# Optimization experiments

Hardware: AMD Instinct MI355X
Metric: run time of the kernel (lower is better)

## Reference

```python
import jax, jax.numpy as jnp
import numpy as np

SAMPLE_RATE = 16000
SOUND_SPEED = 343.0
MAX_ORDER = 15
RIR_LENGTH = 3968
WINDOW_LENGTH = 81
PAD = WINDOW_LENGTH // 2  # 40

# Static image-source lattice (depends only on max_order): all integer
# reflection index triplets with |nx|+|ny|+|nz| <= max_order.
_ind = np.arange(-MAX_ORDER, MAX_ORDER + 1)
_grid = np.stack(np.meshgrid(_ind, _ind, _ind, indexing="ij"), -1).reshape(-1, 3)
XYZ = _grid[np.abs(_grid).sum(1) <= MAX_ORDER].astype(np.float32)  # (I,3), I=4991
EXP_LO = np.abs(np.floor(XYZ / 2)).astype(np.float32)        # hits on lower walls per dim
EXP_HI = np.abs(np.floor((XYZ + 1) / 2)).astype(np.float32)  # hits on upper walls per dim


def _hann(x, T):
    # continuous Hann window sampled at non-integer points, zero outside |x|<=T/2
    return jnp.where(jnp.abs(x) <= T / 2, 0.5 * (1.0 + jnp.cos(2.0 * jnp.pi * x / T)), 0.0)


def _forward(inp):
    room = inp[:, 0:3]                 # (B,3) room dimensions [m]
    mic = inp[:, 3:6] * room           # (B,3)
    src = inp[:, 6:9] * room           # (B,3)
    a_w = inp[:, 9:10]
    absorption = jnp.concatenate([a_w, a_w, a_w, a_w, inp[:, 10:11], inp[:, 11:12]], axis=1)
    absorption = absorption * 0.84 + 0.01            # (B,6): [x-,x+,y-,y+,floor,ceiling]
    tr = jnp.sqrt(1.0 - absorption)                  # wall reflection coefficients

    xyz = jnp.asarray(XYZ)                           # (I,3)
    d = room[:, None, :]
    s = src[:, None, :]
    # image source locations (B,I,3): mirror parity per torchaudio ISM
    img_loc = jnp.where(xyz % 2 == 1, d * (xyz + 1.0) - s, d * xyz + s)
    # per-image-source attenuation (B,I)
    t_lo = tr[:, None, 0::2]                         # (B,1,3) lower walls per dim
    t_hi = tr[:, None, 1::2]                         # (B,1,3) upper walls per dim
    att = jnp.prod(t_lo ** jnp.asarray(EXP_LO) * t_hi ** jnp.asarray(EXP_HI), axis=-1)

    dist = jnp.linalg.norm(img_loc - mic[:, None, :], axis=-1)   # (B,I)
    amp = att / dist                                              # 1/r spreading
    delay = dist * (SAMPLE_RATE / SOUND_SPEED)                    # fractional sample delay
    delay_i = jnp.ceil(delay)

    # windowed-sinc fractional-delay pulse sampled at n = delay_i-PAD .. delay_i+PAD
    n_rel = jnp.arange(-PAD, PAD + 1, dtype=jnp.float32)          # (W,)
    x = delay_i[..., None] + n_rel - delay[..., None]             # (B,I,W)
    sig = amp[..., None] * jnp.sinc(x) * _hann(x, 2 * PAD)        # (B,I,W)

    # scatter-accumulate pulses at time index n, dropping out-of-range samples
    t_idx = (delay_i[..., None] + n_rel).astype(jnp.int32)        # (B,I,W)
    B = inp.shape[0]
    b_idx = jnp.arange(B, dtype=jnp.int32)[:, None, None]
    rir = jnp.zeros((B, RIR_LENGTH), dtype=sig.dtype).at[b_idx, t_idx].add(sig, mode="drop")

    toa = PAD + SAMPLE_RATE * jnp.linalg.norm(mic - src, axis=1) / SOUND_SPEED  # (B,)
    return rir, toa


def setup_inputs():
    key = jax.random.key(0)
    u = jax.random.uniform(key, (128, 12), dtype=jnp.float32)
    room = 2.0 + 8.0 * u[:, :3]          # room dims in [2,10] m
    rest = 0.05 + 0.9 * u[:, 3:]         # mic/src fractions and absorptions in (0,1)
    return {"input": jnp.concatenate([room, rest], axis=1)}


def reference(input):
    return _forward(input)
```

## Files before the change

### kernel.cpp

```cpp
#include <hip/hip_runtime.h>

#define NIMG    4991
#define RIRLEN  3968
#define NT      512
#define NGRP    8
#define KPT     10
#define INV_PI  0.31830988618379067f
#define SR_OVER_C 46.647230320699704f

struct Tab { int v[NIMG]; };
static constexpr Tab make_tab() {
    Tab t{};
    int k = 0;
    for (int x = -15; x <= 15; ++x)
        for (int y = -15; y <= 15; ++y)
            for (int z = -15; z <= 15; ++z) {
                int ax = x < 0 ? -x : x;
                int ay = y < 0 ? -y : y;
                int az = z < 0 ? -z : z;
                if (ax + ay + az <= 15)
                    t.v[k++] = (x + 15) | ((y + 15) << 8) | ((z + 15) << 16);
            }
    return t;
}
__constant__ Tab c_tab = make_tab();

static __device__ __forceinline__ int iabs(int v) { return v < 0 ? -v : v; }

typedef __fp16 f16x2 __attribute__((ext_vector_type(2)));

__global__ __launch_bounds__(NT, 4)
void rir_fused(const float* __restrict__ inp, float* __restrict__ out, int B) {
    const int bx   = blockIdx.x;
    const int b    = bx >> 3;
    const int g    = bx & 7;
    const int tid  = threadIdx.x;
    const int lane = tid & 63;
    const int wv   = tid >> 6;
    const int q    = lane & 3;

    __shared__ __align__(16) float2   s_dh[NIMG];
    __shared__ __align__(16) unsigned s_cs[NIMG];
    __shared__ float    s_par[12];
    __shared__ float    s_p2[3][32];
    __shared__ float    s_at[3][32];
    __shared__ int      s_h4[256][4];
    __shared__ int      s_off[257];
    __shared__ float    s_acc[8][64];

    for (int k = tid; k < 1024; k += NT) ((int*)s_h4)[k] = 0;
    if (tid < 512) ((float*)s_acc)[tid] = 0.0f;
    if (tid == 0) {
        const float* ip = inp + b * 12;
        float rx = ip[0], ry = ip[1], rz = ip[2];
        float mx = ip[3] * rx, my = ip[4] * ry, mz = ip[5] * rz;
        float sx = ip[6] * rx, sy = ip[7] * ry, sz = ip[8] * rz;
        float aw = __builtin_fmaf(ip[9],  0.84f, 0.01f);
        float a4 = __builtin_fmaf(ip[10], 0.84f, 0.01f);
        float a5 = __builtin_fmaf(ip[11], 0.84f, 0.01f);
        s_par[0] = rx; s_par[1] = ry; s_par[2] = rz;
        s_par[3] = mx; s_par[4] = my; s_par[5] = mz;
        s_par[6] = sx; s_par[7] = sy; s_par[8] = sz;
        s_par[9]  = 0.5f * __builtin_amdgcn_logf(1.0f - aw);
        s_par[10] = 0.5f * __builtin_amdgcn_logf(1.0f - a4);
        s_par[11] = 0.5f * __builtin_amdgcn_logf(1.0f - a5);
        if (g == 0) {
            float dx = mx - sx, dy = my - sy, dz = mz - sz;
            out[(size_t)B * RIRLEN + b] = __builtin_fmaf(
                __builtin_sqrtf(dx * dx + dy * dy + dz * dz), SR_OVER_C, 40.0f);
        }
    }
    __syncthreads();

    if (tid < 96) {
        const int axis = tid >> 5;
        const int j    = tid & 31;
        if (j < 31) {
            const int n = j - 15;
            const float rr = s_par[axis];
            const float mm = s_par[3 + axis];
            const float ss = s_par[6 + axis];
            const float iv = (n & 1) ? __builtin_fmaf(rr, (float)(n + 1), -ss)
                                     : __builtin_fmaf(rr, (float)n, ss);
            const float pv = iv - mm;
            s_p2[axis][j] = pv * pv;
            const float e4 = (float)iabs(n >> 1);
            const float e5 = (float)iabs((n + 1) >> 1);
            const float ex = (axis < 2)
                ? (e4 + e5) * s_par[9]
                : __builtin_fmaf(e4, s_par[10], e5 * s_par[11]);
            s_at[axis][j] = __builtin_amdgcn_exp2f(ex);
        }
    }
    __syncthreads();

    const int fb = (4 * g + 1) & 31;

    float2   edh[KPT];
    unsigned ecs[KPT];
    int      enc[KPT];
    #pragma unroll
    for (int k = 0; k < KPT; ++k) {
        enc[k] = -1;
        const int idx = tid + k * NT;
        if (idx < NIMG) {
            const int p  = c_tab.v[idx];
            const int xi = p & 255;
            const int yi = (p >> 8) & 255;
            const int zi = (p >> 16) & 255;
            const float d2   = s_p2[0][xi] + s_p2[1][yi] + s_p2[2][zi];
            const float dist = __builtin_sqrtf(d2);
            const float delay = dist * SR_OVER_C;
            const float di    = __builtin_ceilf(delay);
            const int   ti0   = (int)di - 40;
            const int   bk    = (ti0 + 96) >> 4;
            const bool owned  = ((unsigned)((bk - fb + 32) & 31) < 9u);
            if (ti0 < RIRLEN && owned) {
                const float att = s_at[0][xi] * s_at[1][yi] * s_at[2][zi];
                const float amp = att * __builtin_amdgcn_rcpf(dist);
                float frac = di - delay;
                if (frac == 0.0f) frac = di * 1.52587890625e-05f;
                const int dii = (int)di;
                float c1p = amp * __builtin_amdgcn_sinf(0.5f * frac) * INV_PI;
                if (dii & 1) c1p = -c1p;
                const float Hp     = 0.5f * c1p;
                const float dstore = di - frac;
                const float rv = dstore * 0.0125f;
                const float fr = rv - __builtin_floorf(rv);
                const float Hcd = Hp * __builtin_amdgcn_cosf(fr);
                const float Hsd = Hp * __builtin_amdgcn_sinf(fr);
                const f16x2 pk2 = __builtin_amdgcn_cvt_pkrtz(Hcd, Hsd);

                const int rnk = atomicAdd(&s_h4[bk][q], 1);
                enc[k] = (bk << 13) | rnk;
                edh[k] = make_float2(dstore, Hp);
                ecs[k] = __builtin_bit_cast(unsigned, pk2);
            }
        }
    }
    __syncthreads();

    if (wv == 0) {
        const int l = lane;
        const int4 a0 = *(const int4*)&s_h4[4 * l + 0][0];
        const int4 a1 = *(const int4*)&s_h4[4 * l + 1][0];
        const int4 a2 = *(const int4*)&s_h4[4 * l + 2][0];
        const int4 a3 = *(const int4*)&s_h4[4 * l + 3][0];
        const int c0 = a0.x + a0.y + a0.z + a0.w;
        const int c1 = a1.x + a1.y + a1.z + a1.w;
        const int c2 = a2.x + a2.y + a2.z + a2.w;
        const int c3 = a3.x + a3.y + a3.z + a3.w;
        const int ts = c0 + c1 + c2 + c3;
        int incl = ts;
        #pragma unroll
        for (int d = 1; d < 64; d <<= 1) {
            const int u = __shfl_up(incl, d, 64);
            if (l >= d) incl += u;
        }
        const int base = incl - ts;
        s_off[4 * l + 0] = base;
        s_off[4 * l + 1] = base + c0;
        s_off[4 * l + 2] = base + c0 + c1;
        s_off[4 * l + 3] = base + c0 + c1 + c2;
        if (l == 63) s_off[256] = incl;
    }
    __syncthreads();

    if (tid < 256) {
        int run = s_off[tid];
        #pragma unroll
        for (int p = 0; p < 4; ++p) {
            const int c = s_h4[tid][p];
            s_h4[tid][p] = run;
            run += c;
        }
    }
    __syncthreads();

    #pragma unroll
    for (int k = 0; k < KPT; ++k) {
        if (enc[k] >= 0) {
            const int bk   = enc[k] >> 13;
            const int slot = s_h4[bk][q] + (enc[k] & 8191);
            s_dh[slot] = edh[k];
            s_cs[slot] = ecs[k];
        }
    }
    __syncthreads();

    int wlo[8], wlen[8], wpre[8];
    int T = 0, nw = 0;
    #pragma unroll
    for (int kk = 0; kk < 8; ++kk) {
        const int wi = g + 8 * kk;
        wpre[kk] = T;
        if (wi < 62) {
            wlo[kk]  = s_off[4 * wi + 1];
            wlen[kk] = s_off[4 * wi + 10] - wlo[kk];
            T += wlen[kk];
            nw = kk + 1;
        } else { wlo[kk] = 0; wlen[kk] = 0; }
    }
    const int a0r = (T * wv) >> 3;
    const int a1r = (T * (wv + 1)) >> 3;

#define EV1(ACC, DLY, HPV, PKU) do {                                         \
        const f16x2 hh = __builtin_bit_cast(f16x2, (PKU));                   \
        const float xw = tf - (DLY);                                         \
        const float pre = __builtin_fmaf(cth0, (float)hh.x,                  \
                              __builtin_fmaf(sth0, (float)hh.y, (HPV)));     \
        const float hm = (__builtin_fabsf(xw) <= 40.0f) ? pre : 0.0f;        \
        ACC = __builtin_fmaf(hm, __builtin_amdgcn_rcpf(xw), ACC);            \
    } while (0)

    #pragma unroll
    for (int kk = 0; kk < 8; ++kk) {
        if (wlen[kk] == 0) continue;
        const int o0 = (wpre[kk] > a0r) ? wpre[kk] : a0r;
        const int oe = ((wpre[kk] + wlen[kk]) < a1r) ? (wpre[kk] + wlen[kk]) : a1r;
        if (o0 >= oe) continue;
        int       i  = wlo[kk] + (o0 - wpre[kk]);
        const int ie = wlo[kk] + (oe - wpre[kk]);

        const int   wi   = g + 8 * kk;
        const int   t    = (wi << 6) + lane;
        const float tf   = (float)t;
        const int   m    = t - (t / 80) * 80;
        const float cth0 = __builtin_amdgcn_cosf((float)m * 0.0125f);
        const float sth0 = __builtin_amdgcn_sinf((float)m * 0.0125f);

        float acc0 = 0.0f, acc1 = 0.0f;
        while (i < ie && (i & 3)) { EV1(acc0, s_dh[i].x, s_dh[i].y, s_cs[i]); ++i; }
        for (; i + 8 <= ie; i += 8) {
            const float4 d0 = *(const float4*)&s_dh[i];
            const float4 d1 = *(const float4*)&s_dh[i + 2];
            const float4 d2 = *(const float4*)&s_dh[i + 4];
            const float4 d3 = *(const float4*)&s_dh[i + 6];
            const uint4  c0 = *(const uint4*)&s_cs[i];
            const uint4  c1 = *(const uint4*)&s_cs[i + 4];
            EV1(acc0, d0.x, d0.y, c0.x); EV1(acc1, d0.z, d0.w, c0.y);
            EV1(acc0, d1.x, d1.y, c0.z); EV1(acc1, d1.z, d1.w, c0.w);
            EV1(acc0, d2.x, d2.y, c1.x); EV1(acc1, d2.z, d2.w, c1.y);
            EV1(acc0, d3.x, d3.y, c1.z); EV1(acc1, d3.z, d3.w, c1.w);
        }
        for (; i < ie; ++i) EV1(acc0, s_dh[i].x, s_dh[i].y, s_cs[i]);

        atomicAdd(&s_acc[kk][lane], acc0 + acc1);
    }
#undef EV1
    __syncthreads();

    if (tid < 64 * nw) {
        const int kk = tid >> 6;
        const int wi = g + 8 * kk;
        const int t  = (wi << 6) + lane;
        const float sl = (lane & 1) ? -1.0f : 1.0f;
        out[(size_t)b * RIRLEN + t] = sl * s_acc[kk][lane];
    }
}

extern "C" void kernel_launch(void* const* d_in, const int* in_sizes, int n_in,
                              void* d_out, int out_size, void* d_ws, size_t ws_size,
                              hipStream_t stream) {
    (void)d_ws; (void)ws_size; (void)n_in; (void)out_size;
    const float* inp = (const float*)d_in[0];
    float* out = (float*)d_out;
    const int B = in_sizes[0] / 12;
    rir_fused<<<dim3(B * NGRP), dim3(NT), 0, stream>>>(inp, out, B);
}
```

Measured before the change: 96.61 us.

## Evaluate two output samples per lane to reuse each loaded pulse

```diff
diff --git a/kernel.cpp b/kernel.cpp
--- a/kernel.cpp
+++ b/kernel.cpp
@@ -46,10 +46,10 @@
     __shared__ float    s_at[3][32];
     __shared__ int      s_h4[256][4];
     __shared__ int      s_off[257];
-    __shared__ float    s_acc[8][64];
+    __shared__ float    s_acc[4][128];
 
     for (int k = tid; k < 1024; k += NT) ((int*)s_h4)[k] = 0;
-    if (tid < 512) ((float*)s_acc)[tid] = 0.0f;
+    ((float*)s_acc)[tid] = 0.0f;
     if (tid == 0) {
         const float* ip = inp + b * 12;
         float rx = ip[0], ry = ip[1], rz = ip[2];
@@ -94,7 +94,7 @@
     }
     __syncthreads();
 
-    const int fb = (4 * g + 1) & 31;
+    const int fb = 8 * g + 1;
 
     float2   edh[KPT];
     unsigned ecs[KPT];
@@ -114,7 +114,7 @@
             const float di    = __builtin_ceilf(delay);
             const int   ti0   = (int)di - 40;
             const int   bk    = (ti0 + 96) >> 4;
-            const bool owned  = ((unsigned)((bk - fb + 32) & 31) < 9u);
+            const bool owned  = ((unsigned)((bk - fb + 64) & 63) < 13u);
             if (ti0 < RIRLEN && owned) {
                 const float att = s_at[0][xi] * s_at[1][yi] * s_at[2][zi];
                 const float amp = att * __builtin_amdgcn_rcpf(dist);
@@ -188,15 +188,15 @@
     }
     __syncthreads();
 
-    int wlo[8], wlen[8], wpre[8];
+    int wlo[4], wlen[4], wpre[4];
     int T = 0, nw = 0;
     #pragma unroll
-    for (int kk = 0; kk < 8; ++kk) {
+    for (int kk = 0; kk < 4; ++kk) {
         const int wi = g + 8 * kk;
         wpre[kk] = T;
-        if (wi < 62) {
-            wlo[kk]  = s_off[4 * wi + 1];
-            wlen[kk] = s_off[4 * wi + 10] - wlo[kk];
+        if (wi < 31) {
+            wlo[kk]  = s_off[8 * wi + 1];
+            wlen[kk] = s_off[8 * wi + 14] - wlo[kk];
             T += wlen[kk];
             nw = kk + 1;
         } else { wlo[kk] = 0; wlen[kk] = 0; }
@@ -204,17 +204,23 @@
     const int a0r = (T * wv) >> 3;
     const int a1r = (T * (wv + 1)) >> 3;
 
-#define EV1(ACC, DLY, HPV, PKU) do {                                         \
+#define EV2(DLY, HPV, PKU) do {                                              \
         const f16x2 hh = __builtin_bit_cast(f16x2, (PKU));                   \
-        const float xw = tf - (DLY);                                         \
-        const float pre = __builtin_fmaf(cth0, (float)hh.x,                  \
-                              __builtin_fmaf(sth0, (float)hh.y, (HPV)));     \
-        const float hm = (__builtin_fabsf(xw) <= 40.0f) ? pre : 0.0f;        \
-        ACC = __builtin_fmaf(hm, __builtin_amdgcn_rcpf(xw), ACC);            \
+        const float hx = (float)hh.x, hy = (float)hh.y;                      \
+        const float xa = tfa - (DLY);                                        \
+        const float xb = xa + 64.0f;                                         \
+        const float pa = __builtin_fmaf(ctha, hx,                            \
+                             __builtin_fmaf(stha, hy, (HPV)));               \
+        const float pb = __builtin_fmaf(cthb, hx,                            \
+                             __builtin_fmaf(sthb, hy, (HPV)));               \
+        const float ha = (__builtin_fabsf(xa) <= 40.0f) ? pa : 0.0f;         \
+        const float hb = (__builtin_fabsf(xb) <= 40.0f) ? pb : 0.0f;         \
+        accA = __builtin_fmaf(ha, __builtin_amdgcn_rcpf(xa), accA);          \
+        accB = __builtin_fmaf(hb, __builtin_amdgcn_rcpf(xb), accB);          \
     } while (0)
 
     #pragma unroll
-    for (int kk = 0; kk < 8; ++kk) {
+    for (int kk = 0; kk < 4; ++kk) {
         if (wlen[kk] == 0) continue;
         const int o0 = (wpre[kk] > a0r) ? wpre[kk] : a0r;
         const int oe = ((wpre[kk] + wlen[kk]) < a1r) ? (wpre[kk] + wlen[kk]) : a1r;
@@ -223,39 +229,39 @@
         const int ie = wlo[kk] + (oe - wpre[kk]);
 
         const int   wi   = g + 8 * kk;
-        const int   t    = (wi << 6) + lane;
-        const float tf   = (float)t;
-        const int   m    = t - (t / 80) * 80;
-        const float cth0 = __builtin_amdgcn_cosf((float)m * 0.0125f);
-        const float sth0 = __builtin_amdgcn_sinf((float)m * 0.0125f);
-
-        float acc0 = 0.0f, acc1 = 0.0f;
-        while (i < ie && (i & 3)) { EV1(acc0, s_dh[i].x, s_dh[i].y, s_cs[i]); ++i; }
-        for (; i + 8 <= ie; i += 8) {
+        const int   t    = (wi << 7) + lane;
+        const float tfa  = (float)t;
+        const int   ma   = t - (t / 80) * 80;
+        const int   mb   = (t + 64) - ((t + 64) / 80) * 80;
+        const float ctha = __builtin_amdgcn_cosf((float)ma * 0.0125f);
+        const float stha = __builtin_amdgcn_sinf((float)ma * 0.0125f);
+        const float cthb = __builtin_amdgcn_cosf((float)mb * 0.0125f);
+        const float sthb = __builtin_amdgcn_sinf((float)mb * 0.0125f);
+
+        float accA = 0.0f, accB = 0.0f;
+        while (i < ie && (i & 3)) { EV2(s_dh[i].x, s_dh[i].y, s_cs[i]); ++i; }
+        for (; i + 4 <= ie; i += 4) {
             const float4 d0 = *(const float4*)&s_dh[i];
             const float4 d1 = *(const float4*)&s_dh[i + 2];
-            const float4 d2 = *(const float4*)&s_dh[i + 4];
-            const float4 d3 = *(const float4*)&s_dh[i + 6];
-            const uint4  c0 = *(const uint4*)&s_cs[i];
-            const uint4  c1 = *(const uint4*)&s_cs[i + 4];
-            EV1(acc0, d0.x, d0.y, c0.x); EV1(acc1, d0.z, d0.w, c0.y);
-            EV1(acc0, d1.x, d1.y, c0.z); EV1(acc1, d1.z, d1.w, c0.w);
-            EV1(acc0, d2.x, d2.y, c1.x); EV1(acc1, d2.z, d2.w, c1.y);
-            EV1(acc0, d3.x, d3.y, c1.z); EV1(acc1, d3.z, d3.w, c1.w);
-        }
-        for (; i < ie; ++i) EV1(acc0, s_dh[i].x, s_dh[i].y, s_cs[i]);
-
-        atomicAdd(&s_acc[kk][lane], acc0 + acc1);
-    }
-#undef EV1
-    __syncthreads();
-
-    if (tid < 64 * nw) {
-        const int kk = tid >> 6;
-        const int wi = g + 8 * kk;
-        const int t  = (wi << 6) + lane;
-        const float sl = (lane & 1) ? -1.0f : 1.0f;
-        out[(size_t)b * RIRLEN + t] = sl * s_acc[kk][lane];
+            const uint4  cc = *(const uint4*)&s_cs[i];
+            EV2(d0.x, d0.y, cc.x); EV2(d0.z, d0.w, cc.y);
+            EV2(d1.x, d1.y, cc.z); EV2(d1.z, d1.w, cc.w);
+        }
+        for (; i < ie; ++i) EV2(s_dh[i].x, s_dh[i].y, s_cs[i]);
+
+        atomicAdd(&s_acc[kk][lane],      accA);
+        atomicAdd(&s_acc[kk][lane + 64], accB);
+    }
+#undef EV2
+    __syncthreads();
+
+    if (tid < 128 * nw) {
+        const int kk  = tid >> 7;
+        const int pos = tid & 127;
+        const int wi  = g + 8 * kk;
+        const int t   = (wi << 7) + pos;
+        const float sl = (t & 1) ? -1.0f : 1.0f;
+        out[(size_t)b * RIRLEN + t] = sl * s_acc[kk][pos];
     }
 }
 
```

New measurement: 103.1 us. 1.07x slower.
